# Optimization experiments

Hardware: AMD Instinct MI355X
Metric: run time of the kernel (lower is better)

Reference implementation:

```python
import jax, jax.numpy as jnp
import numpy as np
import math

B, S, D, H, FF = 8, 1024, 1024, 16, 4096
DH = D // H
EPS = 1e-5


def _layernorm(x, g, b):
    mu = jnp.mean(x, axis=-1, keepdims=True)
    var = jnp.mean((x - mu) ** 2, axis=-1, keepdims=True)
    return (x - mu) * jax.lax.rsqrt(var + EPS) * g + b


def _gelu_tanh(x):
    c = math.sqrt(2.0 / math.pi)
    return 0.5 * x * (1.0 + jnp.tanh(c * (x + 0.044715 * x ** 3)))


def setup_inputs() -> dict:
    key = jax.random.key(0)
    ks = jax.random.split(key, 8)
    s = lambda d: 1.0 / math.sqrt(d)
    return {
        "x": jax.random.normal(ks[0], (B, S, D), jnp.float32),
        "ln1_g": jnp.ones((D,), jnp.float32),
        "ln1_b": jnp.zeros((D,), jnp.float32),
        "w_qkv": jax.random.normal(ks[1], (3 * D, D), jnp.float32) * s(D),
        "b_qkv": jax.random.normal(ks[2], (3 * D,), jnp.float32) * 0.02,
        "w_o": jax.random.normal(ks[3], (D, D), jnp.float32) * s(D),
        "b_o": jax.random.normal(ks[4], (D,), jnp.float32) * 0.02,
        "ln2_g": jnp.ones((D,), jnp.float32),
        "ln2_b": jnp.zeros((D,), jnp.float32),
        "w1": jax.random.normal(ks[5], (FF, D), jnp.float32) * s(D),
        "b1": jax.random.normal(ks[6], (FF,), jnp.float32) * 0.02,
        "w2": jax.random.normal(ks[7], (D, FF), jnp.float32) * s(FF),
        "b2": jnp.zeros((D,), jnp.float32),
    }


def reference(x, ln1_g, ln1_b, w_qkv, b_qkv, w_o, b_o, ln2_g, ln2_b, w1, b1, w2, b2):
    # --- pre-LN causal self-attention ---
    h = _layernorm(x, ln1_g, ln1_b)
    qkv = h @ w_qkv.T + b_qkv                      # [B,S,3D]
    q, k, v = jnp.split(qkv, 3, axis=-1)
    q = q.reshape(B, S, H, DH)
    k = k.reshape(B, S, H, DH)
    v = v.reshape(B, S, H, DH)
    scores = jnp.einsum("bqhd,bkhd->bhqk", q, k) / math.sqrt(DH)
    causal = jnp.triu(jnp.ones((S, S), jnp.bool_), 1)  # True above diagonal
    scores = jnp.where(causal, -jnp.inf, scores)
    attn = jax.nn.softmax(scores, axis=-1)
    o = jnp.einsum("bhqk,bkhd->bqhd", attn, v).reshape(B, S, D)
    x = x + (o @ w_o.T + b_o)
    # --- FFN ---
    h = _layernorm(x, ln2_g, ln2_b)
    h = _gelu_tanh(h @ w1.T + b1) @ w2.T + b2
    return x + h
```

## Files before the change

kernel.cpp:

```cpp
#include <hip/hip_runtime.h>
#include <math.h>


typedef __bf16 bf16_t;
typedef __bf16 bf16x4 __attribute__((ext_vector_type(4)));
typedef __bf16 bf16x8 __attribute__((ext_vector_type(8)));
typedef float f32x4 __attribute__((ext_vector_type(4)));

#define WAITVM(N) asm volatile("s_waitcnt vmcnt(" #N ")" ::: "memory")
#define WAITLGKM0 asm volatile("s_waitcnt lgkmcnt(0)" ::: "memory")
#define SCHEDBAR __builtin_amdgcn_sched_barrier(0)

__device__ __forceinline__ void async16(const void* g, void* l) {
    __builtin_amdgcn_global_load_lds(
        (const __attribute__((address_space(1))) void*)g,
        (__attribute__((address_space(3))) void*)l,
        16, 0, 0);
}

__device__ __forceinline__ void ln_row(const float* __restrict__ x,
                                       const float* __restrict__ g,
                                       const float* __restrict__ bb,
                                       bf16_t* __restrict__ out, int row) {
    const int tid = threadIdx.x;
    const float4 xv = *(const float4*)(x + row * 1024 + tid * 4);
    float s1 = xv.x + xv.y + xv.z + xv.w;
    float s2 = xv.x * xv.x + xv.y * xv.y + xv.z * xv.z + xv.w * xv.w;
#pragma unroll
    for (int m = 32; m >= 1; m >>= 1) {
        s1 += __shfl_xor(s1, m);
        s2 += __shfl_xor(s2, m);
    }
    __shared__ float r1[4], r2[4];
    const int wid = tid >> 6, lane = tid & 63;
    if (lane == 0) { r1[wid] = s1; r2[wid] = s2; }
    __syncthreads();
    s1 = r1[0] + r1[1] + r1[2] + r1[3];
    s2 = r2[0] + r2[1] + r2[2] + r2[3];
    const float mu = s1 * (1.0f / 1024.0f);
    const float var = s2 * (1.0f / 1024.0f) - mu * mu;
    const float rs = rsqrtf(var + 1e-5f);
    const float4 gv = *(const float4*)(g + tid * 4);
    const float4 bv = *(const float4*)(bb + tid * 4);
    bf16x4 o;
    o[0] = (bf16_t)((xv.x - mu) * rs * gv.x + bv.x);
    o[1] = (bf16_t)((xv.y - mu) * rs * gv.y + bv.y);
    o[2] = (bf16_t)((xv.z - mu) * rs * gv.z + bv.z);
    o[3] = (bf16_t)((xv.w - mu) * rs * gv.w + bv.w);
    *(bf16x4*)(out + row * 1024 + tid * 4) = o;
}

__global__ __launch_bounds__(256) void prep(
    const float* __restrict__ s0, const float* __restrict__ s1,
    const float* __restrict__ s2, const float* __restrict__ s3,
    bf16_t* __restrict__ d0, bf16_t* __restrict__ d1,
    bf16_t* __restrict__ d2, bf16_t* __restrict__ d3,
    const float* __restrict__ x, const float* __restrict__ ln1g,
    const float* __restrict__ ln1b, bf16_t* __restrict__ h) {
    if (blockIdx.x >= 12288) {
        ln_row(x, ln1g, ln1b, h, blockIdx.x - 12288);
        return;
    }
    const int g = blockIdx.x * 256 + threadIdx.x;
    const float* s;
    bf16_t* d;
    int off;
    if (g < 786432)       { s = s0; d = d0; off = g; }
    else if (g < 1048576) { s = s1; d = d1; off = g - 786432; }
    else if (g < 2097152) { s = s2; d = d2; off = g - 1048576; }
    else                  { s = s3; d = d3; off = g - 2097152; }
    const int i = off * 4;
    const float4 v = *(const float4*)(s + i);
    bf16x4 o;
    o[0] = (bf16_t)v.x; o[1] = (bf16_t)v.y; o[2] = (bf16_t)v.z; o[3] = (bf16_t)v.w;
    *(bf16x4*)(d + i) = o;
}

__global__ __launch_bounds__(256) void ln_b(const bf16_t* __restrict__ x,
                                            const float* __restrict__ g,
                                            const float* __restrict__ bb,
                                            bf16_t* __restrict__ out) {
    const int tid = threadIdx.x;
    const int row = blockIdx.x;
    const bf16x4 xb = *(const bf16x4*)(x + row * 1024 + tid * 4);
    const float x0 = (float)xb[0], x1 = (float)xb[1], x2 = (float)xb[2], x3 = (float)xb[3];
    float s1 = x0 + x1 + x2 + x3;
    float s2 = x0 * x0 + x1 * x1 + x2 * x2 + x3 * x3;
#pragma unroll
    for (int m = 32; m >= 1; m >>= 1) {
        s1 += __shfl_xor(s1, m);
        s2 += __shfl_xor(s2, m);
    }
    __shared__ float r1[4], r2[4];
    const int wid = tid >> 6, lane = tid & 63;
    if (lane == 0) { r1[wid] = s1; r2[wid] = s2; }
    __syncthreads();
    s1 = r1[0] + r1[1] + r1[2] + r1[3];
    s2 = r2[0] + r2[1] + r2[2] + r2[3];
    const float mu = s1 * (1.0f / 1024.0f);
    const float var = s2 * (1.0f / 1024.0f) - mu * mu;
    const float rs = rsqrtf(var + 1e-5f);
    const float4 gv = *(const float4*)(g + tid * 4);
    const float4 bv = *(const float4*)(bb + tid * 4);
    bf16x4 o;
    o[0] = (bf16_t)((x0 - mu) * rs * gv.x + bv.x);
    o[1] = (bf16_t)((x1 - mu) * rs * gv.y + bv.y);
    o[2] = (bf16_t)((x2 - mu) * rs * gv.z + bv.z);
    o[3] = (bf16_t)((x3 - mu) * rs * gv.w + bv.w);
    *(bf16x4*)(out + row * 1024 + tid * 4) = o;
}

template <int MODE>
__global__ __launch_bounds__(512, 2) void gemm2p(
    const bf16_t* __restrict__ A, const bf16_t* __restrict__ W,
    const float* __restrict__ bias, const float* __restrict__ residf,
    const bf16_t* __restrict__ residb,
    bf16_t* __restrict__ outb, float* __restrict__ outf, int N, int K) {
    __shared__ bf16_t lds[49152];
    const int tid = threadIdx.x;
    const int w = tid >> 6, lane = tid & 63;
    const int l15 = lane & 15, quad = lane >> 4;
    const int wm = (w & 1) * 64;
    const int wc = w >> 1;

    const int nwg = gridDim.x;
    const int wg = (blockIdx.x & 7) * (nwg >> 3) + (blockIdx.x >> 3);
    const int nbn = N >> 8;
    const int per = 8 * nbn;
    const int bm = (wg / per) * 8 + (wg % per) % 8;
    const int bn = (wg % per) / 8;
    const int m0 = bm << 7, n0 = bn << 8;

    const bf16_t* pa[2]; const bf16_t* pb[4];
#pragma unroll
    for (int L = 0; L < 2; L++) {
        const int c = L * 512 + tid, r = c >> 3;
        pa[L] = A + (size_t)(m0 + r) * K + ((c & 7) ^ (r & 7)) * 8;
    }
#pragma unroll
    for (int L = 0; L < 4; L++) {
        const int c = L * 512 + tid, r = c >> 3;
        pb[L] = W + (size_t)(n0 + r) * K + ((c & 7) ^ (r & 7)) * 8;
    }

    const int swz0 = (quad ^ (l15 & 7)) * 8;
    const int swz1 = ((4 + quad) ^ (l15 & 7)) * 8;
    const int fragoffA = wm * 64 + l15 * 64 + swz0;
    const bf16_t* bA0 = lds + fragoffA;
    const bf16_t* bA1 = lds + wm * 64 + l15 * 64 + swz1;
    const bf16_t* bB0 = lds + 8192 + wc * 2048 + l15 * 64 + swz0;
    const bf16_t* bB1 = lds + 8192 + wc * 2048 + l15 * 64 + swz1;
    const bf16_t* cA0 = bA0 + 24576;
    const bf16_t* cA1 = bA1 + 24576;
    const bf16_t* cB0 = bB0 + 24576;
    const bf16_t* cB1 = bB1 + 24576;

    f32x4 acc[4][4] = {};
    bf16x8 af[4][2], bfr[4][2];

    async16(pa[0], lds + w * 512);
    async16(pa[1], lds + 4096 + w * 512);
    async16(pb[0], lds + 8192 + w * 512);
    async16(pb[1], lds + 12288 + w * 512);
    async16(pb[2], lds + 16384 + w * 512);
    async16(pb[3], lds + 20480 + w * 512);
    WAITVM(2);
    __builtin_amdgcn_s_barrier();

    const int NT = K >> 6;
    for (int t = 0; t < NT - 1; ++t) {
        bf16_t* nb = (bf16_t*)(cA0 - fragoffA);
        const int kn = (t + 1) << 6;

#pragma unroll
        for (int i = 0; i < 4; i++) {
            af[i][0] = *(const bf16x8*)(bA0 + i * 1024);
            af[i][1] = *(const bf16x8*)(bA1 + i * 1024);
        }
#pragma unroll
        for (int j = 0; j < 2; j++) {
            bfr[j][0] = *(const bf16x8*)(bB0 + j * 1024);
            bfr[j][1] = *(const bf16x8*)(bB1 + j * 1024);
        }
        async16(pa[0] + kn, nb + w * 512);
        async16(pa[1] + kn, nb + 4096 + w * 512);
        async16(pb[0] + kn, nb + 8192 + w * 512);
        async16(pb[1] + kn, nb + 12288 + w * 512);
        SCHEDBAR;
        __builtin_amdgcn_s_barrier();
        WAITLGKM0;
        SCHEDBAR;
        __builtin_amdgcn_s_setprio(1);
#pragma unroll
        for (int i = 0; i < 4; i++)
#pragma unroll
            for (int j = 0; j < 2; j++)
#pragma unroll
                for (int f = 0; f < 2; f++)
                    acc[i][j] = __builtin_amdgcn_mfma_f32_16x16x32_bf16(af[i][f], bfr[j][f], acc[i][j], 0, 0, 0);
        __builtin_amdgcn_s_setprio(0);
        SCHEDBAR;
        WAITVM(4);
        __builtin_amdgcn_s_barrier();

#pragma unroll
        for (int j = 2; j < 4; j++) {
            bfr[j][0] = *(const bf16x8*)(bB0 + 8192 + (j & 1) * 1024);
            bfr[j][1] = *(const bf16x8*)(bB1 + 8192 + (j & 1) * 1024);
        }
        async16(pb[2] + kn, nb + 16384 + w * 512);
        async16(pb[3] + kn, nb + 20480 + w * 512);
        SCHEDBAR;
        __builtin_amdgcn_s_barrier();
        WAITLGKM0;
        SCHEDBAR;
        __builtin_amdgcn_s_setprio(1);
#pragma unroll
        for (int i = 0; i < 4; i++)
#pragma unroll
            for (int j = 2; j < 4; j++)
#pragma unroll
                for (int f = 0; f < 2; f++)
                    acc[i][j] = __builtin_amdgcn_mfma_f32_16x16x32_bf16(af[i][f], bfr[j][f], acc[i][j], 0, 0, 0);
        __builtin_amdgcn_s_setprio(0);
        SCHEDBAR;
        WAITVM(2);
        __builtin_amdgcn_s_barrier();

        { const bf16_t* s;
          s = bA0; bA0 = cA0; cA0 = s;
          s = bA1; bA1 = cA1; cA1 = s;
          s = bB0; bB0 = cB0; cB0 = s;
          s = bB1; bB1 = cB1; cB1 = s; }
    }

    {
#pragma unroll
        for (int i = 0; i < 4; i++) {
            af[i][0] = *(const bf16x8*)(bA0 + i * 1024);
            af[i][1] = *(const bf16x8*)(bA1 + i * 1024);
        }
#pragma unroll
        for (int j = 0; j < 2; j++) {
            bfr[j][0] = *(const bf16x8*)(bB0 + j * 1024);
            bfr[j][1] = *(const bf16x8*)(bB1 + j * 1024);
        }
        SCHEDBAR;
        __builtin_amdgcn_s_barrier();
        WAITLGKM0;
        SCHEDBAR;
        __builtin_amdgcn_s_setprio(1);
#pragma unroll
        for (int i = 0; i < 4; i++)
#pragma unroll
            for (int j = 0; j < 2; j++)
#pragma unroll
                for (int f = 0; f < 2; f++)
                    acc[i][j] = __builtin_amdgcn_mfma_f32_16x16x32_bf16(af[i][f], bfr[j][f], acc[i][j], 0, 0, 0);
        __builtin_amdgcn_s_setprio(0);
        SCHEDBAR;
        WAITVM(0);
        __builtin_amdgcn_s_barrier();
#pragma unroll
        for (int j = 2; j < 4; j++) {
            bfr[j][0] = *(const bf16x8*)(bB0 + 8192 + (j & 1) * 1024);
            bfr[j][1] = *(const bf16x8*)(bB1 + 8192 + (j & 1) * 1024);
        }
        WAITLGKM0;
        SCHEDBAR;
        __builtin_amdgcn_s_setprio(1);
#pragma unroll
        for (int i = 0; i < 4; i++)
#pragma unroll
            for (int j = 2; j < 4; j++)
#pragma unroll
                for (int f = 0; f < 2; f++)
                    acc[i][j] = __builtin_amdgcn_mfma_f32_16x16x32_bf16(af[i][f], bfr[j][f], acc[i][j], 0, 0, 0);
        __builtin_amdgcn_s_setprio(0);
    }

#pragma unroll
    for (int i = 0; i < 4; i++) {
        const int row0 = m0 + wm + i * 16 + quad * 4;
#pragma unroll
        for (int j = 0; j < 4; j++) {
            const int col = n0 + (j >> 1) * 128 + wc * 32 + (j & 1) * 16 + l15;
            const float bcol = bias[col];
            if (MODE == 4) {
#pragma unroll
                for (int q = 0; q < 4; q++) {
                    const size_t idx = (size_t)(row0 + q) * N + col;
                    outb[idx] = (bf16_t)(acc[i][j][q] + bcol + residf[idx]);
                }
            } else {
#pragma unroll
                for (int q = 0; q < 4; q++) {
                    const size_t idx = (size_t)(row0 + q) * N + col;
                    outf[idx] = acc[i][j][q] + bcol + (float)residb[idx];
                }
            }
        }
    }
}

template <int MODE>
__global__ __launch_bounds__(512, 2) void gemm8(
    const bf16_t* __restrict__ A, const bf16_t* __restrict__ W,
    const float* __restrict__ bias, bf16_t* __restrict__ outb,
    bf16_t* __restrict__ vt, int N, int K) {
    __shared__ bf16_t lds[65536];
    const int tid = threadIdx.x;
    const int w = tid >> 6, lane = tid & 63;
    const int l15 = lane & 15, quad = lane >> 4;
    const int wr = w >> 2, wc = w & 3;

    const int nwg = gridDim.x;
    const int wg = (blockIdx.x & 7) * (nwg >> 3) + (blockIdx.x >> 3);
    const int nbn = N >> 8;
    const int per = 8 * nbn;
    const int bm = (wg / per) * 8 + (wg % per) % 8;
    const int bn = (wg % per) / 8;
    const int m0 = bm << 8, n0 = bn << 8;

    int r_[2], s_[2];
#pragma unroll
    for (int L = 0; L < 2; L++) {
        const int c = L * 512 + tid;
        r_[L] = c >> 3;
        s_[L] = ((c & 7) ^ (r_[L] & 7)) * 8;
    }
    const bf16_t* pa0[2]; const bf16_t* pa1[2];
    const bf16_t* pb0[2]; const bf16_t* pb1[2];
#pragma unroll
    for (int L = 0; L < 2; L++) {
        pa0[L] = A + (size_t)(m0 + r_[L]) * K + s_[L];
        pa1[L] = pa0[L] + (size_t)128 * K;
        pb0[L] = W + (size_t)(n0 + r_[L]) * K + s_[L];
        pb1[L] = pb0[L] + (size_t)128 * K;
    }

    const int fragoff = wr * 4096 + l15 * 64;
    const int swz0 = (quad ^ (l15 & 7)) * 8;
    const int swz1 = ((4 + quad) ^ (l15 & 7)) * 8;
    const bf16_t* bA0 = lds + fragoff + swz0;
    const bf16_t* bA1 = lds + fragoff + swz1;
    const bf16_t* bB0 = lds + 16384 + wc * 2048 + l15 * 64 + swz0;
    const bf16_t* bB1 = lds + 16384 + wc * 2048 + l15 * 64 + swz1;
    const bf16_t* cA0 = bA0 + 32768;
    const bf16_t* cA1 = bA1 + 32768;
    const bf16_t* cB0 = bB0 + 32768;
    const bf16_t* cB1 = bB1 + 32768;

    f32x4 acc[8][4] = {};
    bf16x8 af[4][2], bfr[4][2];

    async16(pa0[0], lds + w * 512);
    async16(pa0[1], lds + 4096 + w * 512);
    async16(pb0[0], lds + 16384 + w * 512);
    async16(pb0[1], lds + 20480 + w * 512);
    async16(pb1[0], lds + 24576 + w * 512);
    async16(pb1[1], lds + 28672 + w * 512);
    async16(pa1[0], lds + 8192 + w * 512);
    async16(pa1[1], lds + 12288 + w * 512);
    WAITVM(4);
    __builtin_amdgcn_s_barrier();

    const int NT = K >> 6;
    for (int t = 0; t < NT - 1; ++t) {
        bf16_t* nb = (bf16_t*)(cA0 - (fragoff + swz0));
        const int kn = (t + 1) << 6;

#pragma unroll
        for (int i = 0; i < 4; i++) {
            af[i][0] = *(const bf16x8*)(bA0 + i * 1024);
            af[i][1] = *(const bf16x8*)(bA1 + i * 1024);
        }
#pragma unroll
        for (int j = 0; j < 2; j++) {
            bfr[j][0] = *(const bf16x8*)(bB0 + j * 1024);
            bfr[j][1] = *(const bf16x8*)(bB1 + j * 1024);
        }
        async16(pa0[0] + kn, nb + w * 512);
        async16(pa0[1] + kn, nb + 4096 + w * 512);
        SCHEDBAR;
        __builtin_amdgcn_s_barrier();
        WAITLGKM0;
        SCHEDBAR;
        __builtin_amdgcn_s_setprio(1);
#pragma unroll
        for (int i = 0; i < 4; i++)
#pragma unroll
            for (int j = 0; j < 2; j++)
#pragma unroll
                for (int f = 0; f < 2; f++)
                    acc[i][j] = __builtin_amdgcn_mfma_f32_16x16x32_bf16(af[i][f], bfr[j][f], acc[i][j], 0, 0, 0);
        __builtin_amdgcn_s_setprio(0);
        SCHEDBAR;
        WAITVM(4);
        __builtin_amdgcn_s_barrier();

#pragma unroll
        for (int j = 2; j < 4; j++) {
            bfr[j][0] = *(const bf16x8*)(bB0 + 8192 + (j & 1) * 1024);
            bfr[j][1] = *(const bf16x8*)(bB1 + 8192 + (j & 1) * 1024);
        }
        async16(pb0[0] + kn, nb + 16384 + w * 512);
        async16(pb0[1] + kn, nb + 20480 + w * 512);
        SCHEDBAR;
        __builtin_amdgcn_s_barrier();
        WAITLGKM0;
        SCHEDBAR;
        __builtin_amdgcn_s_setprio(1);
#pragma unroll
        for (int i = 0; i < 4; i++)
#pragma unroll
            for (int j = 2; j < 4; j++)
#pragma unroll
                for (int f = 0; f < 2; f++)
                    acc[i][j] = __builtin_amdgcn_mfma_f32_16x16x32_bf16(af[i][f], bfr[j][f], acc[i][j], 0, 0, 0);
        __builtin_amdgcn_s_setprio(0);
        SCHEDBAR;
        WAITVM(4);
        __builtin_amdgcn_s_barrier();

#pragma unroll
        for (int i = 0; i < 4; i++) {
            af[i][0] = *(const bf16x8*)(bA0 + 8192 + i * 1024);
            af[i][1] = *(const bf16x8*)(bA1 + 8192 + i * 1024);
        }
        async16(pb1[0] + kn, nb + 24576 + w * 512);
        async16(pb1[1] + kn, nb + 28672 + w * 512);
        SCHEDBAR;
        __builtin_amdgcn_s_barrier();
        WAITLGKM0;
        SCHEDBAR;
        __builtin_amdgcn_s_setprio(1);
#pragma unroll
        for (int i = 0; i < 4; i++)
#pragma unroll
            for (int j = 0; j < 2; j++)
#pragma unroll
                for (int f = 0; f < 2; f++)
                    acc[i + 4][j] = __builtin_amdgcn_mfma_f32_16x16x32_bf16(af[i][f], bfr[j][f], acc[i + 4][j], 0, 0, 0);
        __builtin_amdgcn_s_setprio(0);
        SCHEDBAR;
        __builtin_amdgcn_s_barrier();

        async16(pa1[0] + kn, nb + 8192 + w * 512);
        async16(pa1[1] + kn, nb + 12288 + w * 512);
        SCHEDBAR;
        __builtin_amdgcn_s_setprio(1);
#pragma unroll
        for (int i = 0; i < 4; i++)
#pragma unroll
            for (int j = 2; j < 4; j++)
#pragma unroll
                for (int f = 0; f < 2; f++)
                    acc[i + 4][j] = __builtin_amdgcn_mfma_f32_16x16x32_bf16(af[i][f], bfr[j][f], acc[i + 4][j], 0, 0, 0);
        __builtin_amdgcn_s_setprio(0);
        SCHEDBAR;
        WAITVM(4);
        __builtin_amdgcn_s_barrier();

        { const bf16_t* s;
          s = bA0; bA0 = cA0; cA0 = s;
          s = bA1; bA1 = cA1; cA1 = s;
          s = bB0; bB0 = cB0; cB0 = s;
          s = bB1; bB1 = cB1; cB1 = s; }
    }

    {
#pragma unroll
        for (int i = 0; i < 4; i++) {
            af[i][0] = *(const bf16x8*)(bA0 + i * 1024);
            af[i][1] = *(const bf16x8*)(bA1 + i * 1024);
        }
#pragma unroll
        for (int j = 0; j < 2; j++) {
            bfr[j][0] = *(const bf16x8*)(bB0 + j * 1024);
            bfr[j][1] = *(const bf16x8*)(bB1 + j * 1024);
        }
        SCHEDBAR;
        __builtin_amdgcn_s_barrier();
        WAITLGKM0;
        SCHEDBAR;
        __builtin_amdgcn_s_setprio(1);
#pragma unroll
        for (int i = 0; i < 4; i++)
#pragma unroll
            for (int j = 0; j < 2; j++)
#pragma unroll
                for (int f = 0; f < 2; f++)
                    acc[i][j] = __builtin_amdgcn_mfma_f32_16x16x32_bf16(af[i][f], bfr[j][f], acc[i][j], 0, 0, 0);
        __builtin_amdgcn_s_setprio(0);
        SCHEDBAR;
        WAITVM(2);
        __builtin_amdgcn_s_barrier();
#pragma unroll
        for (int j = 2; j < 4; j++) {
            bfr[j][0] = *(const bf16x8*)(bB0 + 8192 + (j & 1) * 1024);
            bfr[j][1] = *(const bf16x8*)(bB1 + 8192 + (j & 1) * 1024);
        }
        SCHEDBAR;
        __builtin_amdgcn_s_barrier();
        WAITLGKM0;
        SCHEDBAR;
        __builtin_amdgcn_s_setprio(1);
#pragma unroll
        for (int i = 0; i < 4; i++)
#pragma unroll
            for (int j = 2; j < 4; j++)
#pragma unroll
                for (int f = 0; f < 2; f++)
                    acc[i][j] = __builtin_amdgcn_mfma_f32_16x16x32_bf16(af[i][f], bfr[j][f], acc[i][j], 0, 0, 0);
        __builtin_amdgcn_s_setprio(0);
        SCHEDBAR;
        WAITVM(0);
        __builtin_amdgcn_s_barrier();
#pragma unroll
        for (int i = 0; i < 4; i++) {
            af[i][0] = *(const bf16x8*)(bA0 + 8192 + i * 1024);
            af[i][1] = *(const bf16x8*)(bA1 + 8192 + i * 1024);
        }
        WAITLGKM0;
        SCHEDBAR;
        __builtin_amdgcn_s_setprio(1);
#pragma unroll
        for (int i = 0; i < 4; i++)
#pragma unroll
            for (int j = 0; j < 4; j++)
#pragma unroll
                for (int f = 0; f < 2; f++)
                    acc[i + 4][j] = __builtin_amdgcn_mfma_f32_16x16x32_bf16(af[i][f], bfr[j][f], acc[i + 4][j], 0, 0, 0);
        __builtin_amdgcn_s_setprio(0);
    }

#pragma unroll
    for (int i = 0; i < 8; i++) {
        const int row0 = m0 + (i >> 2) * 128 + wr * 64 + (i & 3) * 16 + quad * 4;
#pragma unroll
        for (int j = 0; j < 4; j++) {
            const int col = n0 + (j >> 1) * 128 + wc * 32 + (j & 1) * 16 + l15;
            const float bcol = bias[col];
            float v4[4];
#pragma unroll
            for (int q = 0; q < 4; q++) {
                float v = acc[i][j][q] + bcol;
                if (MODE == 1) {
                    const float u2 = -1.5957691216057308f * (v + 0.044715f * v * v * v);
                    v = v * __builtin_amdgcn_rcpf(1.0f + __expf(u2));
                }
                v4[q] = v;
            }
            if (MODE == 3 && col >= 2048) {
                const int bh = (row0 >> 10) * 16 + ((col - 2048) >> 6);
                const int d = (col - 2048) & 63;
                bf16x4 pk;
#pragma unroll
                for (int q = 0; q < 4; q++) pk[q] = (bf16_t)v4[q];
                *(bf16x4*)(vt + (size_t)bh * 65536 + d * 1024 + (row0 & 1023)) = pk;
            } else {
#pragma unroll
                for (int q = 0; q < 4; q++)
                    outb[(size_t)(row0 + q) * N + col] = (bf16_t)v4[q];
            }
        }
    }
}

__global__ __launch_bounds__(512) void attn_mfma(const bf16_t* __restrict__ qkv,
                                                 const bf16_t* __restrict__ vt,
                                                 bf16_t* __restrict__ o) {
    __shared__ bf16_t Ks[4096];
    __shared__ bf16_t Vs[4096];
    __shared__ bf16_t Ps[8][32][72];
    const int tid = threadIdx.x;
    const int w = tid >> 6;
    const int lane = tid & 63;
    const int l15 = lane & 15;
    const int quad = lane >> 4;
    const int qb = blockIdx.x;
    const int bh = blockIdx.y;
    const int b = bh >> 4, h = bh & 15;

    const int qrow = b * 1024 + qb * 256 + w * 32;

    bf16x8 qf[2][2];
#pragma unroll
    for (int g = 0; g < 2; g++)
#pragma unroll
        for (int f = 0; f < 2; f++) {
            bf16x8 t = *(const bf16x8*)(qkv + (size_t)(qrow + g * 16 + l15) * 3072 + h * 64 + f * 32 + quad * 8);
#pragma unroll
            for (int e = 0; e < 8; e++) t[e] = (bf16_t)((float)t[e] * 0.125f);
            qf[g][f] = t;
        }

    f32x4 Ot[2][4] = {};
    float mrow[2] = {-3.0e38f, -3.0e38f};
    float lrow[2] = {0.0f, 0.0f};

    const int c0 = w * 64 + lane;
    const int r0 = c0 >> 3, g0 = (((c0 & 7) ^ (r0 & 7))) * 8;

    const bf16_t* kbase = qkv + (size_t)(b * 1024) * 3072 + 1024 + h * 64;
    const bf16_t* vbase = vt + (size_t)bh * 64 * 1024;

    const int ktmax = 4 * qb + 3;
    for (int kt = 0; kt <= ktmax; kt++) {
        async16(kbase + (size_t)(kt * 64 + r0) * 3072 + g0, Ks + w * 512);
        async16(vbase + (size_t)r0 * 1024 + kt * 64 + g0, Vs + w * 512);
        __syncthreads();

#pragma unroll
        for (int g = 0; g < 2; g++) {
            const int qmaxw = qb * 256 + w * 32 + g * 16 + 15;
            if (kt * 64 > qmaxw) continue;
            const int ktd = qmaxw >> 6;
            const int kbd = (2 * w + g) & 3;

            f32x4 sf[4];
#pragma unroll
            for (int kb = 0; kb < 4; kb++) {
                if (kt * 64 + kb * 16 > qmaxw) {
                    sf[kb] = (f32x4){-3.0e38f, -3.0e38f, -3.0e38f, -3.0e38f};
                    continue;
                }
                const int r = kb * 16 + l15;
                f32x4 acc = {};
#pragma unroll
                for (int f = 0; f < 2; f++) {
                    const int seg = (f * 4 + quad) ^ (r & 7);
                    const bf16x8 kf = *(const bf16x8*)(Ks + r * 64 + seg * 8);
                    acc = __builtin_amdgcn_mfma_f32_16x16x32_bf16(kf, qf[g][f], acc, 0, 0, 0);
                }
                if (kt == ktd && kb == kbd) {
#pragma unroll
                    for (int rr2 = 0; rr2 < 4; rr2++)
                        if (quad * 4 + rr2 > l15) acc[rr2] = -3.0e38f;
                }
                sf[kb] = acc;
            }

            float tmax = -3.0e38f;
#pragma unroll
            for (int kb = 0; kb < 4; kb++)
#pragma unroll
                for (int rr2 = 0; rr2 < 4; rr2++) tmax = fmaxf(tmax, sf[kb][rr2]);
            tmax = fmaxf(tmax, __shfl_xor(tmax, 16));
            tmax = fmaxf(tmax, __shfl_xor(tmax, 32));
            const float mnew = fmaxf(mrow[g], tmax);
            const float alpha = __expf(mrow[g] - mnew);
            float psum = 0.0f;
#pragma unroll
            for (int kb = 0; kb < 4; kb++) {
                bf16x4 pk;
#pragma unroll
                for (int rr2 = 0; rr2 < 4; rr2++) {
                    const float p = __expf(sf[kb][rr2] - mnew);
                    psum += p;
                    pk[rr2] = (bf16_t)p;
                }
                *(bf16x4*)(&Ps[w][g * 16 + l15][kb * 16 + quad * 4]) = pk;
            }
            psum += __shfl_xor(psum, 16);
            psum += __shfl_xor(psum, 32);
            lrow[g] = lrow[g] * alpha + psum;
            mrow[g] = mnew;
#pragma unroll
            for (int db = 0; db < 4; db++)
#pragma unroll
                for (int rr2 = 0; rr2 < 4; rr2++) Ot[g][db][rr2] *= alpha;

#pragma unroll
            for (int ks = 0; ks < 2; ks++) {
                if (kt * 64 + ks * 32 > qmaxw) break;
                const bf16x8 pf = *(const bf16x8*)(&Ps[w][g * 16 + l15][ks * 32 + quad * 8]);
#pragma unroll
                for (int db = 0; db < 4; db++) {
                    const int d = db * 16 + l15;
                    const int seg = (ks * 4 + quad) ^ (d & 7);
                    const bf16x8 vf = *(const bf16x8*)(Vs + d * 64 + seg * 8);
                    Ot[g][db] = __builtin_amdgcn_mfma_f32_16x16x32_bf16(vf, pf, Ot[g][db], 0, 0, 0);
                }
            }
        }
        __syncthreads();
    }

#pragma unroll
    for (int g = 0; g < 2; g++) {
        const float rl = 1.0f / lrow[g];
#pragma unroll
        for (int db = 0; db < 4; db++) {
            bf16x4 ov;
#pragma unroll
            for (int rr2 = 0; rr2 < 4; rr2++) ov[rr2] = (bf16_t)(Ot[g][db][rr2] * rl);
            *(bf16x4*)(o + (size_t)(qrow + g * 16 + l15) * 1024 + h * 64 + db * 16 + quad * 4) = ov;
        }
    }
}

extern "C" void kernel_launch(void* const* d_in, const int* in_sizes, int n_in,
                              void* d_out, int out_size, void* d_ws, size_t ws_size,
                              hipStream_t stream) {
    const float* x     = (const float*)d_in[0];
    const float* ln1g  = (const float*)d_in[1];
    const float* ln1b  = (const float*)d_in[2];
    const float* w_qkv = (const float*)d_in[3];
    const float* b_qkv = (const float*)d_in[4];
    const float* w_o   = (const float*)d_in[5];
    const float* b_o   = (const float*)d_in[6];
    const float* ln2g  = (const float*)d_in[7];
    const float* ln2b  = (const float*)d_in[8];
    const float* w1    = (const float*)d_in[9];
    const float* b1    = (const float*)d_in[10];
    const float* w2    = (const float*)d_in[11];
    const float* b2    = (const float*)d_in[12];
    float* out = (float*)d_out;

    char* w = (char*)d_ws;
    bf16_t* wbqkv = (bf16_t*)(w + 0);
    bf16_t* wbo   = (bf16_t*)(w + 6291456);
    bf16_t* wb1   = (bf16_t*)(w + 8388608);
    bf16_t* wb2   = (bf16_t*)(w + 16777216);
    bf16_t* h     = (bf16_t*)(w + 25165824);
    bf16_t* qkv   = (bf16_t*)(w + 41943040);
    bf16_t* ob    = (bf16_t*)(w + 92274688);
    bf16_t* x1b   = (bf16_t*)(w + 109051904);
    bf16_t* f     = (bf16_t*)(w + 142606336);
    bf16_t* vtb   = (bf16_t*)(w + 142606336);

    prep<<<20480, 256, 0, stream>>>(w_qkv, w_o, w1, w2, wbqkv, wbo, wb1, wb2,
                                    x, ln1g, ln1b, h);
    gemm8<3><<<384, 512, 0, stream>>>(h, wbqkv, b_qkv, qkv, vtb, 3072, 1024);
    attn_mfma<<<dim3(4, 128), 512, 0, stream>>>(qkv, vtb, ob);
    gemm2p<4><<<256, 512, 0, stream>>>(ob, wbo, b_o, x, nullptr, x1b, nullptr, 1024, 1024);
    ln_b<<<8192, 256, 0, stream>>>(x1b, ln2g, ln2b, h);
    gemm8<1><<<512, 512, 0, stream>>>(h, wb1, b1, f, nullptr, 4096, 1024);
    gemm2p<5><<<256, 512, 0, stream>>>(f, wb2, b2, nullptr, x1b, nullptr, out, 1024, 4096);
}
```

Measured before the change: 436.8 us.

## Double-buffer K/V tiles in attention to overlap loads with MFMA compute

The attention kernel now keeps two shared-memory buffers for K and V. It issues the async global-to-LDS load for the next key tile before computing on the current one, and waits on vmcnt plus a single barrier at the end of each iteration. This replaces the per-iteration load-then-sync with one sync per tile and hides load latency behind the QK/PV MFMAs. To offset the doubled K/V LDS footprint, the per-wave P scratch is shrunk to 16 rows and reused across the two query groups.

```diff
diff --git a/kernel.cpp b/kernel.cpp
--- a/kernel.cpp
+++ b/kernel.cpp
@@ -571,9 +571,9 @@
 __global__ __launch_bounds__(512) void attn_mfma(const bf16_t* __restrict__ qkv,
                                                  const bf16_t* __restrict__ vt,
                                                  bf16_t* __restrict__ o) {
-    __shared__ bf16_t Ks[4096];
-    __shared__ bf16_t Vs[4096];
-    __shared__ bf16_t Ps[8][32][72];
+    __shared__ bf16_t Ks[2][4096];
+    __shared__ bf16_t Vs[2][4096];
+    __shared__ bf16_t Ps[8][16][72];
     const int tid = threadIdx.x;
     const int w = tid >> 6;
     const int lane = tid & 63;
@@ -607,10 +607,20 @@
     const bf16_t* vbase = vt + (size_t)bh * 64 * 1024;
 
     const int ktmax = 4 * qb + 3;
-    for (int kt = 0; kt <= ktmax; kt++) {
-        async16(kbase + (size_t)(kt * 64 + r0) * 3072 + g0, Ks + w * 512);
-        async16(vbase + (size_t)r0 * 1024 + kt * 64 + g0, Vs + w * 512);
-        __syncthreads();
+
+    async16(kbase + (size_t)r0 * 3072 + g0, &Ks[0][0] + w * 512);
+    async16(vbase + (size_t)r0 * 1024 + g0, &Vs[0][0] + w * 512);
+    WAITVM(0);
+    __builtin_amdgcn_s_barrier();
+
+    int p = 0;
+    for (int kt = 0; kt <= ktmax; kt++, p ^= 1) {
+        if (kt < ktmax) {
+            async16(kbase + (size_t)((kt + 1) * 64 + r0) * 3072 + g0, &Ks[p ^ 1][0] + w * 512);
+            async16(vbase + (size_t)r0 * 1024 + (kt + 1) * 64 + g0, &Vs[p ^ 1][0] + w * 512);
+        }
+        const bf16_t* Kp = &Ks[p][0];
+        const bf16_t* Vp = &Vs[p][0];
 
 #pragma unroll
         for (int g = 0; g < 2; g++) {
@@ -631,7 +641,7 @@
 #pragma unroll
                 for (int f = 0; f < 2; f++) {
                     const int seg = (f * 4 + quad) ^ (r & 7);
-                    const bf16x8 kf = *(const bf16x8*)(Ks + r * 64 + seg * 8);
+                    const bf16x8 kf = *(const bf16x8*)(Kp + r * 64 + seg * 8);
                     acc = __builtin_amdgcn_mfma_f32_16x16x32_bf16(kf, qf[g][f], acc, 0, 0, 0);
                 }
                 if (kt == ktd && kb == kbd) {
@@ -657,11 +667,11 @@
                 bf16x4 pk;
 #pragma unroll
                 for (int rr2 = 0; rr2 < 4; rr2++) {
-                    const float p = __expf(sf[kb][rr2] - mnew);
-                    psum += p;
-                    pk[rr2] = (bf16_t)p;
+                    const float p2 = __expf(sf[kb][rr2] - mnew);
+                    psum += p2;
+                    pk[rr2] = (bf16_t)p2;
                 }
-                *(bf16x4*)(&Ps[w][g * 16 + l15][kb * 16 + quad * 4]) = pk;
+                *(bf16x4*)(&Ps[w][l15][kb * 16 + quad * 4]) = pk;
             }
             psum += __shfl_xor(psum, 16);
             psum += __shfl_xor(psum, 32);
@@ -675,17 +685,19 @@
 #pragma unroll
             for (int ks = 0; ks < 2; ks++) {
                 if (kt * 64 + ks * 32 > qmaxw) break;
-                const bf16x8 pf = *(const bf16x8*)(&Ps[w][g * 16 + l15][ks * 32 + quad * 8]);
+                const bf16x8 pf = *(const bf16x8*)(&Ps[w][l15][ks * 32 + quad * 8]);
 #pragma unroll
                 for (int db = 0; db < 4; db++) {
                     const int d = db * 16 + l15;
                     const int seg = (ks * 4 + quad) ^ (d & 7);
-                    const bf16x8 vf = *(const bf16x8*)(Vs + d * 64 + seg * 8);
+                    const bf16x8 vf = *(const bf16x8*)(Vp + d * 64 + seg * 8);
                     Ot[g][db] = __builtin_amdgcn_mfma_f32_16x16x32_bf16(vf, pf, Ot[g][db], 0, 0, 0);
                 }
             }
         }
-        __syncthreads();
+        SCHEDBAR;
+        WAITVM(0);
+        __builtin_amdgcn_s_barrier();
     }
 
 #pragma unroll
```

New measurement: 438.4 us. About the same (+0.4%).
